# Kernel optimization log

Measured on AMD Instinct MI355X. Metric: run time of the kernel, lower is better.

## Reference

```python
import jax, jax.numpy as jnp
import numpy as np

B, N, H = 1, 512, 768  # batch, seq_len (incl. BOS/EOS), encoder_embed_dim


def setup_inputs() -> dict:
    key = jax.random.key(0)
    k1, k2 = jax.random.split(key, 2)
    inputs = jax.random.normal(k1, (B, N, H), dtype=jnp.float32)
    # Linear(2H -> 2): weight [2, 2H], bias [2]
    W = jax.random.normal(k2, (2, 2 * H), dtype=jnp.float32) * (1.0 / np.sqrt(2 * H)).astype(np.float32)
    b = jnp.zeros((2,), dtype=jnp.float32)
    return {"inputs": inputs, "W": W, "b": b}


def reference(inputs, W, b):
    # Pairwise features: prod and diff, each [B, N, N, H].
    # Linear on concat(prod, diff) == prod @ W1^T + diff @ W2^T (avoids materializing the concat).
    Hd = inputs.shape[-1]
    W1, W2 = W[:, :Hd], W[:, Hd:]
    prod = inputs[:, :, None, :] * inputs[:, None, :, :]
    diff = inputs[:, :, None, :] - inputs[:, None, :, :]
    pred = (jnp.einsum('bijh,oh->bijo', prod, W1)
            + jnp.einsum('bijh,oh->bijo', diff, W2)
            + b)  # [B, N, N, 2]
    # Symmetrize over the two sequence axes, then drop BOS/EOS positions.
    pred = (pred + pred.transpose(0, 2, 1, 3)) * 0.5
    return pred[:, 1:-1, 1:-1]  # [B, N-2, N-2, 2]
```

## Files before the change

### kernel.cpp

```cpp
#include <hip/hip_runtime.h>
#include <hip/hip_bf16.h>


constexpr int H   = 768;
constexpr int M   = 510;
constexpr int BK  = 256;
constexpr int NST = H / BK;
constexpr int LDP = BK + 8;

typedef __attribute__((ext_vector_type(8))) short short8;
typedef __attribute__((ext_vector_type(4))) float f32x4;

__device__ inline void cvt_store4(unsigned short* p, float4 v) {
  __hip_bfloat162 lo = __float22bfloat162_rn(make_float2(v.x, v.y));
  __hip_bfloat162 hi = __float22bfloat162_rn(make_float2(v.z, v.w));
  uint2 u;
  u.x = *(unsigned int*)&lo;
  u.y = *(unsigned int*)&hi;
  *(uint2*)p = u;
}

__device__ inline float4 mul4(float4 a, float4 b) {
  return make_float4(a.x * b.x, a.y * b.y, a.z * b.z, a.w * b.w);
}

__global__ __launch_bounds__(256, 1) void pairwise_head_mfma(
    const float* __restrict__ X, const float* __restrict__ W,
    const float* __restrict__ bias, float* __restrict__ out) {
  __shared__ __align__(16) unsigned short sm[3 * 32 * LDP];
  unsigned short* sA0 = sm;
  unsigned short* sA1 = sm + 32 * LDP;
  unsigned short* sB  = sm + 2 * 32 * LDP;

  const int tid = threadIdx.x;
  const int gi0 = blockIdx.y * 32;
  const int gj0 = blockIdx.x * 32;

  const int srow  = tid >> 3;
  const int scol8 = tid & 7;
  int arow = gi0 + 1 + srow; if (arow > 511) arow = 511;
  int brow = gj0 + 1 + srow; if (brow > 511) brow = 511;
  const float4* Xa = (const float4*)(X + (size_t)arow * H);
  const float4* Xb = (const float4*)(X + (size_t)brow * H);
  const float4* W0 = (const float4*)(W);
  const float4* W1 = (const float4*)(W + 1536);

  const int wave = tid >> 6;
  const int lane = tid & 63;
  const int lo = lane & 15;
  const int q  = lane >> 4;
  const int mi = wave >> 1;
  const int nj = wave & 1;
  const unsigned short* pa0 = sA0 + (mi * 16 + lo) * LDP + q * 8;
  const unsigned short* pa1 = sA1 + (mi * 16 + lo) * LDP + q * 8;
  const unsigned short* pb  = sB  + (nj * 16 + lo) * LDP + q * 8;

  f32x4 acc0 = {0.f, 0.f, 0.f, 0.f};
  f32x4 acc1 = {0.f, 0.f, 0.f, 0.f};

  float4 px[8], py[8], pw0[8], pw1[8];
#pragma unroll
  for (int s = 0; s < 8; ++s) {
    const int c = scol8 + 8 * s;
    px[s] = Xa[c]; py[s] = Xb[c]; pw0[s] = W0[c]; pw1[s] = W1[c];
  }

#pragma unroll
  for (int st = 0; st < NST; ++st) {
    if (st > 0) __syncthreads();
#pragma unroll
    for (int s = 0; s < 8; ++s) {
      const int c = scol8 + 8 * s;
      cvt_store4(sA0 + srow * LDP + 4 * c, mul4(px[s], pw0[s]));
      cvt_store4(sA1 + srow * LDP + 4 * c, mul4(px[s], pw1[s]));
      cvt_store4(sB  + srow * LDP + 4 * c, py[s]);
    }
    __syncthreads();

    if (st + 1 < NST) {
      const int g4 = (st + 1) * (BK / 4);
#pragma unroll
      for (int s = 0; s < 8; ++s) {
        const int c = g4 + scol8 + 8 * s;
        px[s] = Xa[c]; py[s] = Xb[c]; pw0[s] = W0[c]; pw1[s] = W1[c];
      }
    }

#pragma unroll
    for (int c = 0; c < BK / 32; ++c) {
      const short8 a0 = *(const short8*)(pa0 + c * 32);
      const short8 a1 = *(const short8*)(pa1 + c * 32);
      const short8 b  = *(const short8*)(pb  + c * 32);
      acc0 = __builtin_amdgcn_mfma_f32_16x16x32_bf16(a0, b, acc0, 0, 0, 0);
      acc1 = __builtin_amdgcn_mfma_f32_16x16x32_bf16(a1, b, acc1, 0, 0, 0);
    }
  }

  const float b0 = bias[0];
  const float b1 = bias[1];
  const int j  = gj0 + nj * 16 + lo;
  const int i0 = gi0 + mi * 16 + q * 4;
  if (j < M) {
#pragma unroll
    for (int r = 0; r < 4; ++r) {
      const int i = i0 + r;
      if (i < M) {
        float2 v = make_float2(acc0[r] + b0, acc1[r] + b1);
        *(float2*)(out + ((size_t)i * M + j) * 2) = v;
      }
    }
  }
}

extern "C" void kernel_launch(void* const* d_in, const int* in_sizes, int n_in,
                              void* d_out, int out_size, void* d_ws, size_t ws_size,
                              hipStream_t stream) {
  const float* X    = (const float*)d_in[0];
  const float* W    = (const float*)d_in[1];
  const float* bias = (const float*)d_in[2];
  float* out = (float*)d_out;

  dim3 grid(16, 16);
  dim3 block(256);
  hipLaunchKernelGGL(pairwise_head_mfma, grid, block, 0, stream,
                     X, W, bias, out);
}
```

Baseline: 61.88 us.

## Stage full K in LDS and split K across two wave groups with LDS reduction

Each block now has 512 threads and loads the whole 768-wide K dimension into shared memory in one pass, replacing the three-stage loop and its per-stage barriers. The eight waves split K in half: each 16x16 output tile is computed by two waves, and their partial sums are combined through shared memory before the store. This removes the serial staged pipeline and doubles the number of waves available to hide latency. In exchange it uses much more LDS per block, adds a reduction step with two extra barriers, and the whole load completes before any MFMA work starts.

```diff
diff --git a/kernel.cpp b/kernel.cpp
--- a/kernel.cpp
+++ b/kernel.cpp
@@ -4,9 +4,7 @@
 
 constexpr int H   = 768;
 constexpr int M   = 510;
-constexpr int BK  = 256;
-constexpr int NST = H / BK;
-constexpr int LDP = BK + 8;
+constexpr int LDP = H + 8;
 
 typedef __attribute__((ext_vector_type(8))) short short8;
 typedef __attribute__((ext_vector_type(4))) float f32x4;
@@ -24,7 +22,7 @@
   return make_float4(a.x * b.x, a.y * b.y, a.z * b.z, a.w * b.w);
 }
 
-__global__ __launch_bounds__(256, 1) void pairwise_head_mfma(
+__global__ __launch_bounds__(512, 1) void pairwise_head_mfma(
     const float* __restrict__ X, const float* __restrict__ W,
     const float* __restrict__ bias, float* __restrict__ out) {
   __shared__ __align__(16) unsigned short sm[3 * 32 * LDP];
@@ -36,77 +34,85 @@
   const int gi0 = blockIdx.y * 32;
   const int gj0 = blockIdx.x * 32;
 
-  const int srow  = tid >> 3;
-  const int scol8 = tid & 7;
+  const int srow = tid >> 4;
+  const int sc   = tid & 15;
   int arow = gi0 + 1 + srow; if (arow > 511) arow = 511;
   int brow = gj0 + 1 + srow; if (brow > 511) brow = 511;
   const float4* Xa = (const float4*)(X + (size_t)arow * H);
   const float4* Xb = (const float4*)(X + (size_t)brow * H);
   const float4* W0 = (const float4*)(W);
   const float4* W1 = (const float4*)(W + 1536);
+  unsigned short* a0p = sA0 + srow * LDP + sc * 4;
+  unsigned short* a1p = sA1 + srow * LDP + sc * 4;
+  unsigned short* bp  = sB  + srow * LDP + sc * 4;
+
+#pragma unroll
+  for (int u = 0; u < 6; ++u) {
+    const int cl = u * 32 + sc;
+    float4 xa0 = Xa[cl], xa1 = Xa[cl + 16];
+    float4 xb0 = Xb[cl], xb1 = Xb[cl + 16];
+    float4 w00 = W0[cl], w01 = W0[cl + 16];
+    float4 w10 = W1[cl], w11 = W1[cl + 16];
+    cvt_store4(a0p + u * 128,      mul4(xa0, w00));
+    cvt_store4(a0p + u * 128 + 64, mul4(xa1, w01));
+    cvt_store4(a1p + u * 128,      mul4(xa0, w10));
+    cvt_store4(a1p + u * 128 + 64, mul4(xa1, w11));
+    cvt_store4(bp  + u * 128,      xb0);
+    cvt_store4(bp  + u * 128 + 64, xb1);
+  }
+  __syncthreads();
 
   const int wave = tid >> 6;
   const int lane = tid & 63;
   const int lo = lane & 15;
   const int q  = lane >> 4;
-  const int mi = wave >> 1;
-  const int nj = wave & 1;
-  const unsigned short* pa0 = sA0 + (mi * 16 + lo) * LDP + q * 8;
-  const unsigned short* pa1 = sA1 + (mi * 16 + lo) * LDP + q * 8;
-  const unsigned short* pb  = sB  + (nj * 16 + lo) * LDP + q * 8;
+  const int quad = wave & 3;
+  const int kh   = wave >> 2;
+  const int mi = quad >> 1;
+  const int nj = quad & 1;
+  const unsigned short* pa0 = sA0 + (mi * 16 + lo) * LDP + kh * 384 + q * 8;
+  const unsigned short* pa1 = sA1 + (mi * 16 + lo) * LDP + kh * 384 + q * 8;
+  const unsigned short* pb  = sB  + (nj * 16 + lo) * LDP + kh * 384 + q * 8;
 
   f32x4 acc0 = {0.f, 0.f, 0.f, 0.f};
   f32x4 acc1 = {0.f, 0.f, 0.f, 0.f};
-
-  float4 px[8], py[8], pw0[8], pw1[8];
 #pragma unroll
-  for (int s = 0; s < 8; ++s) {
-    const int c = scol8 + 8 * s;
-    px[s] = Xa[c]; py[s] = Xb[c]; pw0[s] = W0[c]; pw1[s] = W1[c];
+  for (int c = 0; c < 12; ++c) {
+    const short8 a0 = *(const short8*)(pa0 + c * 32);
+    const short8 a1 = *(const short8*)(pa1 + c * 32);
+    const short8 b  = *(const short8*)(pb  + c * 32);
+    acc0 = __builtin_amdgcn_mfma_f32_16x16x32_bf16(a0, b, acc0, 0, 0, 0);
+    acc1 = __builtin_amdgcn_mfma_f32_16x16x32_bf16(a1, b, acc1, 0, 0, 0);
   }
 
+  __syncthreads();
+
+  float* red = (float*)sm;
+  if (kh == 1) {
 #pragma unroll
-  for (int st = 0; st < NST; ++st) {
-    if (st > 0) __syncthreads();
-#pragma unroll
-    for (int s = 0; s < 8; ++s) {
-      const int c = scol8 + 8 * s;
-      cvt_store4(sA0 + srow * LDP + 4 * c, mul4(px[s], pw0[s]));
-      cvt_store4(sA1 + srow * LDP + 4 * c, mul4(px[s], pw1[s]));
-      cvt_store4(sB  + srow * LDP + 4 * c, py[s]);
-    }
-    __syncthreads();
-
-    if (st + 1 < NST) {
-      const int g4 = (st + 1) * (BK / 4);
-#pragma unroll
-      for (int s = 0; s < 8; ++s) {
-        const int c = g4 + scol8 + 8 * s;
-        px[s] = Xa[c]; py[s] = Xb[c]; pw0[s] = W0[c]; pw1[s] = W1[c];
-      }
-    }
-
-#pragma unroll
-    for (int c = 0; c < BK / 32; ++c) {
-      const short8 a0 = *(const short8*)(pa0 + c * 32);
-      const short8 a1 = *(const short8*)(pa1 + c * 32);
-      const short8 b  = *(const short8*)(pb  + c * 32);
-      acc0 = __builtin_amdgcn_mfma_f32_16x16x32_bf16(a0, b, acc0, 0, 0, 0);
-      acc1 = __builtin_amdgcn_mfma_f32_16x16x32_bf16(a1, b, acc1, 0, 0, 0);
+    for (int r = 0; r < 4; ++r) {
+      const int rl = q * 4 + r;
+      float2 v = make_float2(acc0[r], acc1[r]);
+      *(float2*)(red + ((quad * 16 + rl) * 17 + lo) * 2) = v;
     }
   }
+  __syncthreads();
 
-  const float b0 = bias[0];
-  const float b1 = bias[1];
-  const int j  = gj0 + nj * 16 + lo;
-  const int i0 = gi0 + mi * 16 + q * 4;
-  if (j < M) {
+  if (kh == 0) {
+    const float b0 = bias[0];
+    const float b1 = bias[1];
+    const int j  = gj0 + nj * 16 + lo;
+    const int i0 = gi0 + mi * 16 + q * 4;
+    if (j < M) {
 #pragma unroll
-    for (int r = 0; r < 4; ++r) {
-      const int i = i0 + r;
-      if (i < M) {
-        float2 v = make_float2(acc0[r] + b0, acc1[r] + b1);
-        *(float2*)(out + ((size_t)i * M + j) * 2) = v;
+      for (int r = 0; r < 4; ++r) {
+        const int i = i0 + r;
+        if (i < M) {
+          const float2 p =
+              *(const float2*)(red + ((quad * 16 + (q * 4 + r)) * 17 + lo) * 2);
+          float2 v = make_float2(acc0[r] + p.x + b0, acc1[r] + p.y + b1);
+          *(float2*)(out + ((size_t)i * M + j) * 2) = v;
+        }
       }
     }
   }
@@ -121,7 +127,7 @@
   float* out = (float*)d_out;
 
   dim3 grid(16, 16);
-  dim3 block(256);
+  dim3 block(512);
   hipLaunchKernelGGL(pairwise_head_mfma, grid, block, 0, stream,
                      X, W, bias, out);
 }
```

Result: no change. 62.18 us (+0.5%).
